# Performance work log

Measured on AMD Instinct MI355X. Metric: run time of the kernel, lower is better.

## Reference

```python
import jax, jax.numpy as jnp
import numpy as np

B, N, K, DIN, H = 8, 5000, 16, 128, 128


def setup_inputs() -> dict:
    key = jax.random.key(0)
    ks = jax.random.split(key, 10)
    x = jax.random.normal(ks[0], (B, N, DIN), dtype=jnp.float32)
    neighbor_index = jax.random.randint(ks[1], (N, K), 0, N, dtype=jnp.int32)
    neighbor_weights = jax.random.uniform(ks[2], (N, K), dtype=jnp.float32)
    s = 1.0 / np.sqrt(H)
    W_ih = jax.random.uniform(ks[3], (4 * H, DIN), minval=-s, maxval=s, dtype=jnp.float32)
    W_hh = jax.random.uniform(ks[4], (4 * H, H), minval=-s, maxval=s, dtype=jnp.float32)
    b_ih = jax.random.uniform(ks[5], (4 * H,), minval=-s, maxval=s, dtype=jnp.float32)
    b_hh = jax.random.uniform(ks[6], (4 * H,), minval=-s, maxval=s, dtype=jnp.float32)
    W_self = jax.random.normal(ks[7], (H, DIN), dtype=jnp.float32) * 0.05
    b_self = jnp.zeros((H,), dtype=jnp.float32)
    W_comb = jax.random.normal(ks[8], (H, 2 * H), dtype=jnp.float32) * 0.05
    b_comb = jnp.zeros((H,), dtype=jnp.float32)
    return {"x": x, "neighbor_index": neighbor_index, "neighbor_weights": neighbor_weights,
            "W_ih": W_ih, "W_hh": W_hh, "b_ih": b_ih, "b_hh": b_hh,
            "W_self": W_self, "b_self": b_self, "W_comb": W_comb, "b_comb": b_comb}


def _lstm_last_h(seq, W_ih, W_hh, b_ih, b_hh):
    # seq: (M, K, DIN) -> final hidden state (M, H). PyTorch gate order: i, f, g, o.
    M = seq.shape[0]
    x_gates = jnp.einsum('mkd,gd->mkg', seq, W_ih) + b_ih  # (M, K, 4H)
    x_gates = jnp.swapaxes(x_gates, 0, 1)  # (K, M, 4H)

    def step(carry, xg):
        h, c = carry
        gates = xg + h @ W_hh.T + b_hh
        i, f, g, o = jnp.split(gates, 4, axis=-1)
        i = jax.nn.sigmoid(i); f = jax.nn.sigmoid(f); g = jnp.tanh(g); o = jax.nn.sigmoid(o)
        c = f * c + i * g
        h = o * jnp.tanh(c)
        return (h, c), None

    h0 = jnp.zeros((M, W_hh.shape[0] // 4), dtype=seq.dtype)
    (h, _), _ = jax.lax.scan(step, (h0, h0), x_gates)
    return h


def reference(x, neighbor_index, neighbor_weights, W_ih, W_hh, b_ih, b_hh, W_self, b_self, W_comb, b_comb):
    b, n, din = x.shape
    k = neighbor_index.shape[1]
    # gather neighbor feats: (B, N, K, DIN)
    neigh = jnp.take(x, neighbor_index, axis=1)
    neigh = neigh * neighbor_weights[None, :, :, None]
    lstm_in = neigh.reshape(b * n, k, din)
    agg = _lstm_last_h(lstm_in, W_ih, W_hh, b_ih, b_hh).reshape(b, n, -1)
    self_feats = x @ W_self.T + b_self
    combined = jnp.concatenate([self_feats, agg], axis=-1)
    out = jax.nn.relu(combined @ W_comb.T + b_comb)
    return out
```

## Files before the change

kernel.cpp:

```cpp
#include <hip/hip_runtime.h>
#include <math.h>

#define Bx   8
#define Nx   5000
#define Kx   16
#define DINx 128
#define Hx   128
#define G4x  512
#define Mx   40000

typedef __attribute__((ext_vector_type(8))) short sh8;
typedef __attribute__((ext_vector_type(4))) float f32x4;

__device__ __forceinline__ float sigf(float v) {
    return __fdividef(1.0f, 1.0f + __expf(-v));
}
__device__ __forceinline__ float tanf_(float v) {
    return 1.0f - __fdividef(2.0f, __expf(2.0f * v) + 1.0f);
}
__device__ __forceinline__ unsigned short rne16(float f) {
    unsigned int u = __float_as_uint(f);
    return (unsigned short)((u + 0x7fffu + ((u >> 16) & 1u)) >> 16);
}
__device__ __forceinline__ float b2f(unsigned short s) {
    return __uint_as_float(((unsigned int)s) << 16);
}

#define FMA4(P, A, Q)                                        \
    P = fmaf((A).x, (Q).x, P); P = fmaf((A).y, (Q).y, P);    \
    P = fmaf((A).z, (Q).z, P); P = fmaf((A).w, (Q).w, P);

__global__ __launch_bounds__(128) void ka(const float* __restrict__ x,
        const float* __restrict__ W_ih, const float* __restrict__ W_self,
        const float* __restrict__ b_self, float* __restrict__ G,
        float* __restrict__ S)
{
    __shared__ float xs[8 * DINx];
    const int m0 = blockIdx.x * 8;
    {
        const float4* src = (const float4*)(x + (size_t)m0 * DINx);
        float4* dst = (float4*)xs;
        #pragma unroll
        for (int i = 0; i < 2; ++i)
            dst[threadIdx.x + 128 * i] = src[threadIdx.x + 128 * i];
    }
    __syncthreads();

    const int t = threadIdx.x;
    const float4* wp[5];
    #pragma unroll
    for (int c = 0; c < 5; ++c) {
        const int o = t + 128 * c;
        wp[c] = (const float4*)((o < G4x) ? (W_ih + (size_t)o * DINx)
                                          : (W_self + (size_t)(o - G4x) * DINx));
    }
    float acc[8][5];
    #pragma unroll
    for (int n = 0; n < 8; ++n)
        #pragma unroll
        for (int c = 0; c < 5; ++c) acc[n][c] = 0.f;

    #pragma unroll 4
    for (int k4 = 0; k4 < 32; ++k4) {
        float4 wv[5];
        #pragma unroll
        for (int c = 0; c < 5; ++c) wv[c] = wp[c][k4];
        #pragma unroll
        for (int n = 0; n < 8; ++n) {
            const float4 xv = ((const float4*)(xs + n * DINx))[k4];
            #pragma unroll
            for (int c = 0; c < 5; ++c) { FMA4(acc[n][c], xv, wv[c]); }
        }
    }
    const float bs = b_self[t];
    #pragma unroll
    for (int n = 0; n < 8; ++n) {
        const size_t m = (size_t)(m0 + n);
        #pragma unroll
        for (int c = 0; c < 4; ++c)
            G[m * G4x + t + 128 * c] = acc[n][c];
        S[m * Hx + t] = acc[n][4] + bs;
    }
}

__global__ __launch_bounds__(256) void kw(const float* __restrict__ W_hh,
        const float* __restrict__ b_ih, const float* __restrict__ b_hh,
        unsigned short* __restrict__ WH, unsigned short* __restrict__ WL,
        float* __restrict__ bsum)
{
    const int i = blockIdx.x * 256 + threadIdx.x;
    if (i < G4x * Hx) {
        const float w = W_hh[i];
        const unsigned short hi = rne16(w);
        WH[i] = hi;
        WL[i] = rne16(w - b2f(hi));
    }
    if (i < G4x) bsum[i] = b_ih[i] + b_hh[i];
}

__global__ __launch_bounds__(256) void kb(const float* __restrict__ G,
        const float* __restrict__ S, const unsigned short* __restrict__ WH,
        const unsigned short* __restrict__ WL, const float* __restrict__ bsum,
        const int* __restrict__ nidx, const float* __restrict__ nw,
        const float* __restrict__ W_comb, const float* __restrict__ b_comb,
        float* __restrict__ out)
{
    __shared__ unsigned short hsHI[32 * 128];
    __shared__ unsigned short hsLO[32 * 128];
    __shared__ float hsF[32 * 136];
    __shared__ int   gofs[16 * 32];
    __shared__ float wts [16 * 32];

    const int tid    = threadIdx.x;
    const int lane   = tid & 63;
    const int v      = tid >> 6;
    const int row16  = lane & 15;
    const int quad   = lane >> 4;
    const int swzkey = row16 & 7;
    const int dimb   = v * 32;
    const int m0     = blockIdx.x * 32;

    for (int i = tid; i < 512; i += 256) {
        const int s = i & 31, kk = i >> 5;
        const int m = m0 + s;
        const int bb = m / Nx;
        const int nn = m - bb * Nx;
        gofs[kk * 32 + s] = (bb * Nx + nidx[nn * Kx + kk]) * G4x;
        wts [kk * 32 + s] = nw[nn * Kx + kk];
    }
    float bsv[4][2];
    #pragma unroll
    for (int g = 0; g < 4; ++g)
        #pragma unroll
        for (int b2 = 0; b2 < 2; ++b2)
            bsv[g][b2] = bsum[g * 128 + dimb + 16 * b2 + row16];

    float cst[2][2][4];
    #pragma unroll
    for (int mt = 0; mt < 2; ++mt)
        #pragma unroll
        for (int b2 = 0; b2 < 2; ++b2)
            #pragma unroll
            for (int j = 0; j < 4; ++j) cst[mt][b2][j] = 0.f;

    __syncthreads();

    #pragma unroll 1
    for (int k = 0; k < Kx; ++k) {
        float wkv[2][4];
        const float* gp[2][4];
        #pragma unroll
        for (int mt = 0; mt < 2; ++mt)
            #pragma unroll
            for (int j = 0; j < 4; ++j) {
                const int seq = mt * 16 + quad * 4 + j;
                wkv[mt][j] = wts[k * 32 + seq];
                gp[mt][j]  = G + gofs[k * 32 + seq] + dimb + row16;
            }
        float gld[2][4][4][2];
        #pragma unroll
        for (int mt = 0; mt < 2; ++mt)
            #pragma unroll
            for (int j = 0; j < 4; ++j)
                #pragma unroll
                for (int g = 0; g < 4; ++g)
                    #pragma unroll
                    for (int b2 = 0; b2 < 2; ++b2)
                        gld[mt][j][g][b2] = gp[mt][j][(g << 7) + (b2 << 4)];

        f32x4 acc[2][4][2];
        #pragma unroll
        for (int mt = 0; mt < 2; ++mt)
            #pragma unroll
            for (int g = 0; g < 4; ++g)
                #pragma unroll
                for (int b2 = 0; b2 < 2; ++b2)
                    acc[mt][g][b2] = (f32x4)0.f;

        if (k) {
            #pragma unroll
            for (int kt = 0; kt < 4; ++kt) {
                sh8 ahi[2], alo[2];
                #pragma unroll
                for (int mt = 0; mt < 2; ++mt) {
                    const int ro = ((mt * 16 + row16) << 7) +
                                   ((((kt << 2) + quad) ^ swzkey) << 3);
                    ahi[mt] = *(const sh8*)(hsHI + ro);
                    alo[mt] = *(const sh8*)(hsLO + ro);
                }
                #pragma unroll
                for (int b2 = 0; b2 < 2; ++b2) {
                    #pragma unroll
                    for (int g = 0; g < 4; ++g) {
                        const int nro = ((g << 7) + dimb + (b2 << 4) + row16) * 128
                                        + (kt << 5) + (quad << 3);
                        const sh8 wh = *(const sh8*)(WH + nro);
                        const sh8 wl = *(const sh8*)(WL + nro);
                        #pragma unroll
                        for (int mt = 0; mt < 2; ++mt) {
                            acc[mt][g][b2] = __builtin_amdgcn_mfma_f32_16x16x32_bf16(
                                ahi[mt], wh, acc[mt][g][b2], 0, 0, 0);
                            acc[mt][g][b2] = __builtin_amdgcn_mfma_f32_16x16x32_bf16(
                                alo[mt], wh, acc[mt][g][b2], 0, 0, 0);
                            acc[mt][g][b2] = __builtin_amdgcn_mfma_f32_16x16x32_bf16(
                                ahi[mt], wl, acc[mt][g][b2], 0, 0, 0);
                        }
                    }
                }
            }
        }

        float hval[2][2][4];
        #pragma unroll
        for (int mt = 0; mt < 2; ++mt)
            #pragma unroll
            for (int b2 = 0; b2 < 2; ++b2)
                #pragma unroll
                for (int j = 0; j < 4; ++j) {
                    const float pi = acc[mt][0][b2][j] + wkv[mt][j] * gld[mt][j][0][b2] + bsv[0][b2];
                    const float pf = acc[mt][1][b2][j] + wkv[mt][j] * gld[mt][j][1][b2] + bsv[1][b2];
                    const float pg = acc[mt][2][b2][j] + wkv[mt][j] * gld[mt][j][2][b2] + bsv[2][b2];
                    const float po = acc[mt][3][b2][j] + wkv[mt][j] * gld[mt][j][3][b2] + bsv[3][b2];
                    const float ig = sigf(pi), fg = sigf(pf);
                    const float gg = tanf_(pg), og = sigf(po);
                    const float cc = fg * cst[mt][b2][j] + ig * gg;
                    cst[mt][b2][j] = cc;
                    hval[mt][b2][j] = og * tanf_(cc);
                }

        __syncthreads();

        if (k < Kx - 1) {
            #pragma unroll
            for (int mt = 0; mt < 2; ++mt)
                #pragma unroll
                for (int b2 = 0; b2 < 2; ++b2)
                    #pragma unroll
                    for (int j = 0; j < 4; ++j) {
                        const int seq = mt * 16 + quad * 4 + j;
                        const int dim = dimb + (b2 << 4) + row16;
                        const int idx = (seq << 7) +
                                        ((((dim >> 3) ^ (seq & 7))) << 3) + (dim & 7);
                        const float f = hval[mt][b2][j];
                        const unsigned short hi = rne16(f);
                        hsHI[idx] = hi;
                        hsLO[idx] = rne16(f - b2f(hi));
                    }
        } else {
            #pragma unroll
            for (int mt = 0; mt < 2; ++mt)
                #pragma unroll
                for (int b2 = 0; b2 < 2; ++b2)
                    #pragma unroll
                    for (int j = 0; j < 4; ++j) {
                        const int seq = mt * 16 + quad * 4 + j;
                        const int dim = dimb + (b2 << 4) + row16;
                        hsF[seq * 136 + dim] = hval[mt][b2][j];
                    }
        }
        __syncthreads();
    }

    const int dg = tid & 31;
    const int sg = tid >> 5;
    float ac[4][4];
    #pragma unroll
    for (int i = 0; i < 4; ++i)
        #pragma unroll
        for (int j = 0; j < 4; ++j) ac[i][j] = 0.f;

    const float4* S4 = (const float4*)S;
    const float4* W4 = (const float4*)W_comb;
    #pragma unroll 4
    for (int d4 = 0; d4 < 32; ++d4) {
        float4 sv[4], wv[4];
        #pragma unroll
        for (int i = 0; i < 4; ++i)
            sv[i] = S4[(size_t)(m0 + sg * 4 + i) * 32 + d4];
        #pragma unroll
        for (int j = 0; j < 4; ++j) wv[j] = W4[(dg * 4 + j) * 64 + d4];
        #pragma unroll
        for (int i = 0; i < 4; ++i) {
            #pragma unroll
            for (int j = 0; j < 4; ++j) { FMA4(ac[i][j], sv[i], wv[j]); }
        }
    }
    #pragma unroll 4
    for (int d4 = 0; d4 < 32; ++d4) {
        float4 hv[4], wv[4];
        #pragma unroll
        for (int i = 0; i < 4; ++i)
            hv[i] = *(const float4*)(hsF + (sg * 4 + i) * 136 + d4 * 4);
        #pragma unroll
        for (int j = 0; j < 4; ++j) wv[j] = W4[(dg * 4 + j) * 64 + 32 + d4];
        #pragma unroll
        for (int i = 0; i < 4; ++i) {
            #pragma unroll
            for (int j = 0; j < 4; ++j) { FMA4(ac[i][j], hv[i], wv[j]); }
        }
    }
    const float4 bc = ((const float4*)b_comb)[dg];
    #pragma unroll
    for (int i = 0; i < 4; ++i) {
        float4 o4;
        o4.x = fmaxf(ac[i][0] + bc.x, 0.f);
        o4.y = fmaxf(ac[i][1] + bc.y, 0.f);
        o4.z = fmaxf(ac[i][2] + bc.z, 0.f);
        o4.w = fmaxf(ac[i][3] + bc.w, 0.f);
        *(float4*)(out + (size_t)(m0 + sg * 4 + i) * 128 + dg * 4) = o4;
    }
}

extern "C" void kernel_launch(void* const* d_in, const int* in_sizes, int n_in,
                              void* d_out, int out_size, void* d_ws, size_t ws_size,
                              hipStream_t stream)
{
    const float* x      = (const float*)d_in[0];
    const int*   nidx   = (const int*)  d_in[1];
    const float* nw     = (const float*)d_in[2];
    const float* W_ih   = (const float*)d_in[3];
    const float* W_hh   = (const float*)d_in[4];
    const float* b_ih   = (const float*)d_in[5];
    const float* b_hh   = (const float*)d_in[6];
    const float* W_self = (const float*)d_in[7];
    const float* b_self = (const float*)d_in[8];
    const float* W_comb = (const float*)d_in[9];
    const float* b_comb = (const float*)d_in[10];
    float* out = (float*)d_out;

    float* G = (float*)d_ws;
    float* S = G + (size_t)Mx * G4x;
    unsigned short* WH = (unsigned short*)(S + (size_t)Mx * Hx);
    unsigned short* WL = WH + (size_t)G4x * Hx;
    float* bsum = (float*)(WL + (size_t)G4x * Hx);

    kw<<<(G4x * Hx + 255) / 256, 256, 0, stream>>>(W_hh, b_ih, b_hh, WH, WL, bsum);
    ka<<<Mx / 8, 128, 0, stream>>>(x, W_ih, W_self, b_self, G, S);
    kb<<<Mx / 32, 256, 0, stream>>>(G, S, WH, WL, bsum, nidx, nw,
                                    W_comb, b_comb, out);
}
```

Measured before the change: 1.423 ms.

## Prepack W_hh fragments, transpose MFMA operands, vectorize gathers and enlarge projection tile

Packs the split bf16 W_hh into a lane-contiguous fragment layout so each wave loads weight fragments with one coalesced 16-byte read per lane. The MFMA operands are swapped so the output tile becomes dims×sequences. This lets gate pre-activations be gathered as float4 and folded with bias into the accumulator initialisation. Hidden state is written back to LDS as ushort4, shared memory is overlaid into one buffer, and launch bounds ask for 3 blocks per CU. The input projection kernel also processes 16 rows per block instead of 8, which reuses weights more but raises register pressure.

```diff
diff --git a/kernel.cpp b/kernel.cpp
--- a/kernel.cpp
+++ b/kernel.cpp
@@ -35,13 +35,13 @@
         const float* __restrict__ b_self, float* __restrict__ G,
         float* __restrict__ S)
 {
-    __shared__ float xs[8 * DINx];
-    const int m0 = blockIdx.x * 8;
+    __shared__ float xs[16 * DINx];
+    const int m0 = blockIdx.x * 16;
     {
         const float4* src = (const float4*)(x + (size_t)m0 * DINx);
         float4* dst = (float4*)xs;
         #pragma unroll
-        for (int i = 0; i < 2; ++i)
+        for (int i = 0; i < 4; ++i)
             dst[threadIdx.x + 128 * i] = src[threadIdx.x + 128 * i];
     }
     __syncthreads();
@@ -54,19 +54,19 @@
         wp[c] = (const float4*)((o < G4x) ? (W_ih + (size_t)o * DINx)
                                           : (W_self + (size_t)(o - G4x) * DINx));
     }
-    float acc[8][5];
-    #pragma unroll
-    for (int n = 0; n < 8; ++n)
+    float acc[16][5];
+    #pragma unroll
+    for (int n = 0; n < 16; ++n)
         #pragma unroll
         for (int c = 0; c < 5; ++c) acc[n][c] = 0.f;
 
-    #pragma unroll 4
+    #pragma unroll 2
     for (int k4 = 0; k4 < 32; ++k4) {
         float4 wv[5];
         #pragma unroll
         for (int c = 0; c < 5; ++c) wv[c] = wp[c][k4];
         #pragma unroll
-        for (int n = 0; n < 8; ++n) {
+        for (int n = 0; n < 16; ++n) {
             const float4 xv = ((const float4*)(xs + n * DINx))[k4];
             #pragma unroll
             for (int c = 0; c < 5; ++c) { FMA4(acc[n][c], xv, wv[c]); }
@@ -74,7 +74,7 @@
     }
     const float bs = b_self[t];
     #pragma unroll
-    for (int n = 0; n < 8; ++n) {
+    for (int n = 0; n < 16; ++n) {
         const size_t m = (size_t)(m0 + n);
         #pragma unroll
         for (int c = 0; c < 4; ++c)
@@ -85,178 +85,174 @@
 
 __global__ __launch_bounds__(256) void kw(const float* __restrict__ W_hh,
         const float* __restrict__ b_ih, const float* __restrict__ b_hh,
-        unsigned short* __restrict__ WH, unsigned short* __restrict__ WL,
+        unsigned short* __restrict__ WHp, unsigned short* __restrict__ WLp,
         float* __restrict__ bsum)
 {
     const int i = blockIdx.x * 256 + threadIdx.x;
     if (i < G4x * Hx) {
+        const int gdim = i >> 7, kcol = i & 127;
         const float w = W_hh[i];
         const unsigned short hi = rne16(w);
-        WH[i] = hi;
-        WL[i] = rne16(w - b2f(hi));
+        const unsigned short lo = rne16(w - b2f(hi));
+        const int dg16 = gdim >> 4, r16 = gdim & 15;
+        const int kt = kcol >> 5, quad = (kcol >> 3) & 3, e = kcol & 7;
+        const int pidx = (((dg16 * 4 + kt) * 64) + quad * 16 + r16) * 8 + e;
+        WHp[pidx] = hi;
+        WLp[pidx] = lo;
     }
     if (i < G4x) bsum[i] = b_ih[i] + b_hh[i];
 }
 
-__global__ __launch_bounds__(256) void kb(const float* __restrict__ G,
-        const float* __restrict__ S, const unsigned short* __restrict__ WH,
-        const unsigned short* __restrict__ WL, const float* __restrict__ bsum,
+__global__ __launch_bounds__(256, 3) void kb(const float* __restrict__ G,
+        const float* __restrict__ S, const unsigned short* __restrict__ WHp,
+        const unsigned short* __restrict__ WLp, const float* __restrict__ bsum,
         const int* __restrict__ nidx, const float* __restrict__ nw,
         const float* __restrict__ W_comb, const float* __restrict__ b_comb,
         float* __restrict__ out)
 {
-    __shared__ unsigned short hsHI[32 * 128];
-    __shared__ unsigned short hsLO[32 * 128];
-    __shared__ float hsF[32 * 136];
-    __shared__ int   gofs[16 * 32];
-    __shared__ float wts [16 * 32];
-
-    const int tid    = threadIdx.x;
-    const int lane   = tid & 63;
-    const int v      = tid >> 6;
-    const int row16  = lane & 15;
-    const int quad   = lane >> 4;
-    const int swzkey = row16 & 7;
-    const int dimb   = v * 32;
-    const int m0     = blockIdx.x * 32;
+    __shared__ __align__(16) char smem[23552];
+    unsigned short* hsHI = (unsigned short*)smem;
+    unsigned short* hsLO = (unsigned short*)(smem + 8192);
+    float*          hsF  = (float*)smem;
+    int*            gofs = (int*)(smem + 17408);
+    float*          wts  = (float*)(smem + 17408 + 2048);
+    float*          biasL= (float*)(smem + 17408 + 4096);
+
+    const int tid   = threadIdx.x;
+    const int lane  = tid & 63;
+    const int v     = tid >> 6;
+    const int row16 = lane & 15;
+    const int quad  = lane >> 4;
+    const int kk    = row16 & 7;
+    const int dimb  = v * 32;
+    const int m0    = blockIdx.x * 32;
 
     for (int i = tid; i < 512; i += 256) {
-        const int s = i & 31, kk = i >> 5;
+        const int s = i & 31, kstep = i >> 5;
         const int m = m0 + s;
         const int bb = m / Nx;
         const int nn = m - bb * Nx;
-        gofs[kk * 32 + s] = (bb * Nx + nidx[nn * Kx + kk]) * G4x;
-        wts [kk * 32 + s] = nw[nn * Kx + kk];
-    }
-    float bsv[4][2];
-    #pragma unroll
-    for (int g = 0; g < 4; ++g)
-        #pragma unroll
-        for (int b2 = 0; b2 < 2; ++b2)
-            bsv[g][b2] = bsum[g * 128 + dimb + 16 * b2 + row16];
+        gofs[kstep * 32 + s] = (bb * Nx + nidx[nn * Kx + kstep]) * G4x;
+        wts [kstep * 32 + s] = nw[nn * Kx + kstep];
+    }
+    biasL[tid]       = bsum[tid];
+    biasL[tid + 256] = bsum[tid + 256];
 
     float cst[2][2][4];
     #pragma unroll
-    for (int mt = 0; mt < 2; ++mt)
-        #pragma unroll
-        for (int b2 = 0; b2 < 2; ++b2)
-            #pragma unroll
-            for (int j = 0; j < 4; ++j) cst[mt][b2][j] = 0.f;
+    for (int st = 0; st < 2; ++st)
+        #pragma unroll
+        for (int dt = 0; dt < 2; ++dt)
+            #pragma unroll
+            for (int j = 0; j < 4; ++j) cst[st][dt][j] = 0.f;
 
     __syncthreads();
 
     #pragma unroll 1
     for (int k = 0; k < Kx; ++k) {
-        float wkv[2][4];
-        const float* gp[2][4];
-        #pragma unroll
-        for (int mt = 0; mt < 2; ++mt)
-            #pragma unroll
-            for (int j = 0; j < 4; ++j) {
-                const int seq = mt * 16 + quad * 4 + j;
-                wkv[mt][j] = wts[k * 32 + seq];
-                gp[mt][j]  = G + gofs[k * 32 + seq] + dimb + row16;
+        const float wk0 = wts[k * 32 + row16];
+        const float wk1 = wts[k * 32 + 16 + row16];
+        const float* g0p = G + gofs[k * 32 + row16] + dimb + quad * 4;
+        const float* g1p = G + gofs[k * 32 + 16 + row16] + dimb + quad * 4;
+
+        f32x4 acc[4][2][2];
+        #pragma unroll
+        for (int g = 0; g < 4; ++g)
+            #pragma unroll
+            for (int dt = 0; dt < 2; ++dt) {
+                const int off = (g << 7) + (dt << 4);
+                const float4 bz = *(const float4*)(biasL + off + dimb + quad * 4);
+                const float4 v0 = *(const float4*)(g0p + off);
+                const float4 v1 = *(const float4*)(g1p + off);
+                acc[g][dt][0][0] = fmaf(wk0, v0.x, bz.x);
+                acc[g][dt][0][1] = fmaf(wk0, v0.y, bz.y);
+                acc[g][dt][0][2] = fmaf(wk0, v0.z, bz.z);
+                acc[g][dt][0][3] = fmaf(wk0, v0.w, bz.w);
+                acc[g][dt][1][0] = fmaf(wk1, v1.x, bz.x);
+                acc[g][dt][1][1] = fmaf(wk1, v1.y, bz.y);
+                acc[g][dt][1][2] = fmaf(wk1, v1.z, bz.z);
+                acc[g][dt][1][3] = fmaf(wk1, v1.w, bz.w);
             }
-        float gld[2][4][4][2];
-        #pragma unroll
-        for (int mt = 0; mt < 2; ++mt)
-            #pragma unroll
-            for (int j = 0; j < 4; ++j)
+
+        if (k) {
+            #pragma unroll
+            for (int kt = 0; kt < 4; ++kt) {
+                const int rsw = (kt * 4 + quad) ^ kk;
+                const sh8 bhi0 = ((const sh8*)hsHI)[row16 * 16 + rsw];
+                const sh8 blo0 = ((const sh8*)hsLO)[row16 * 16 + rsw];
+                const sh8 bhi1 = ((const sh8*)hsHI)[(16 + row16) * 16 + rsw];
+                const sh8 blo1 = ((const sh8*)hsLO)[(16 + row16) * 16 + rsw];
                 #pragma unroll
                 for (int g = 0; g < 4; ++g)
                     #pragma unroll
-                    for (int b2 = 0; b2 < 2; ++b2)
-                        gld[mt][j][g][b2] = gp[mt][j][(g << 7) + (b2 << 4)];
-
-        f32x4 acc[2][4][2];
-        #pragma unroll
-        for (int mt = 0; mt < 2; ++mt)
-            #pragma unroll
-            for (int g = 0; g < 4; ++g)
-                #pragma unroll
-                for (int b2 = 0; b2 < 2; ++b2)
-                    acc[mt][g][b2] = (f32x4)0.f;
-
-        if (k) {
-            #pragma unroll
-            for (int kt = 0; kt < 4; ++kt) {
-                sh8 ahi[2], alo[2];
-                #pragma unroll
-                for (int mt = 0; mt < 2; ++mt) {
-                    const int ro = ((mt * 16 + row16) << 7) +
-                                   ((((kt << 2) + quad) ^ swzkey) << 3);
-                    ahi[mt] = *(const sh8*)(hsHI + ro);
-                    alo[mt] = *(const sh8*)(hsLO + ro);
-                }
-                #pragma unroll
-                for (int b2 = 0; b2 < 2; ++b2) {
-                    #pragma unroll
-                    for (int g = 0; g < 4; ++g) {
-                        const int nro = ((g << 7) + dimb + (b2 << 4) + row16) * 128
-                                        + (kt << 5) + (quad << 3);
-                        const sh8 wh = *(const sh8*)(WH + nro);
-                        const sh8 wl = *(const sh8*)(WL + nro);
-                        #pragma unroll
-                        for (int mt = 0; mt < 2; ++mt) {
-                            acc[mt][g][b2] = __builtin_amdgcn_mfma_f32_16x16x32_bf16(
-                                ahi[mt], wh, acc[mt][g][b2], 0, 0, 0);
-                            acc[mt][g][b2] = __builtin_amdgcn_mfma_f32_16x16x32_bf16(
-                                alo[mt], wh, acc[mt][g][b2], 0, 0, 0);
-                            acc[mt][g][b2] = __builtin_amdgcn_mfma_f32_16x16x32_bf16(
-                                ahi[mt], wl, acc[mt][g][b2], 0, 0, 0);
-                        }
+                    for (int dt = 0; dt < 2; ++dt) {
+                        const int wi = ((g * 8 + v * 2 + dt) * 4 + kt) * 64 + lane;
+                        const sh8 wh = ((const sh8*)WHp)[wi];
+                        const sh8 wl = ((const sh8*)WLp)[wi];
+                        acc[g][dt][0] = __builtin_amdgcn_mfma_f32_16x16x32_bf16(
+                            wh, bhi0, acc[g][dt][0], 0, 0, 0);
+                        acc[g][dt][0] = __builtin_amdgcn_mfma_f32_16x16x32_bf16(
+                            wh, blo0, acc[g][dt][0], 0, 0, 0);
+                        acc[g][dt][0] = __builtin_amdgcn_mfma_f32_16x16x32_bf16(
+                            wl, bhi0, acc[g][dt][0], 0, 0, 0);
+                        acc[g][dt][1] = __builtin_amdgcn_mfma_f32_16x16x32_bf16(
+                            wh, bhi1, acc[g][dt][1], 0, 0, 0);
+                        acc[g][dt][1] = __builtin_amdgcn_mfma_f32_16x16x32_bf16(
+                            wh, blo1, acc[g][dt][1], 0, 0, 0);
+                        acc[g][dt][1] = __builtin_amdgcn_mfma_f32_16x16x32_bf16(
+                            wl, bhi1, acc[g][dt][1], 0, 0, 0);
                     }
-                }
             }
         }
 
-        float hval[2][2][4];
-        #pragma unroll
-        for (int mt = 0; mt < 2; ++mt)
-            #pragma unroll
-            for (int b2 = 0; b2 < 2; ++b2)
+        float hv[2][2][4];
+        #pragma unroll
+        for (int st = 0; st < 2; ++st)
+            #pragma unroll
+            for (int dt = 0; dt < 2; ++dt)
                 #pragma unroll
                 for (int j = 0; j < 4; ++j) {
-                    const float pi = acc[mt][0][b2][j] + wkv[mt][j] * gld[mt][j][0][b2] + bsv[0][b2];
-                    const float pf = acc[mt][1][b2][j] + wkv[mt][j] * gld[mt][j][1][b2] + bsv[1][b2];
-                    const float pg = acc[mt][2][b2][j] + wkv[mt][j] * gld[mt][j][2][b2] + bsv[2][b2];
-                    const float po = acc[mt][3][b2][j] + wkv[mt][j] * gld[mt][j][3][b2] + bsv[3][b2];
-                    const float ig = sigf(pi), fg = sigf(pf);
-                    const float gg = tanf_(pg), og = sigf(po);
-                    const float cc = fg * cst[mt][b2][j] + ig * gg;
-                    cst[mt][b2][j] = cc;
-                    hval[mt][b2][j] = og * tanf_(cc);
+                    const float ig = sigf(acc[0][dt][st][j]);
+                    const float fg = sigf(acc[1][dt][st][j]);
+                    const float gg = tanf_(acc[2][dt][st][j]);
+                    const float og = sigf(acc[3][dt][st][j]);
+                    const float cc = fg * cst[st][dt][j] + ig * gg;
+                    cst[st][dt][j] = cc;
+                    hv[st][dt][j] = og * tanf_(cc);
                 }
 
         __syncthreads();
 
         if (k < Kx - 1) {
             #pragma unroll
-            for (int mt = 0; mt < 2; ++mt)
+            for (int st = 0; st < 2; ++st)
                 #pragma unroll
-                for (int b2 = 0; b2 < 2; ++b2)
-                    #pragma unroll
-                    for (int j = 0; j < 4; ++j) {
-                        const int seq = mt * 16 + quad * 4 + j;
-                        const int dim = dimb + (b2 << 4) + row16;
-                        const int idx = (seq << 7) +
-                                        ((((dim >> 3) ^ (seq & 7))) << 3) + (dim & 7);
-                        const float f = hval[mt][b2][j];
-                        const unsigned short hi = rne16(f);
-                        hsHI[idx] = hi;
-                        hsLO[idx] = rne16(f - b2f(hi));
-                    }
+                for (int dt = 0; dt < 2; ++dt) {
+                    ushort4 shi, slo;
+                    shi.x = rne16(hv[st][dt][0]);
+                    shi.y = rne16(hv[st][dt][1]);
+                    shi.z = rne16(hv[st][dt][2]);
+                    shi.w = rne16(hv[st][dt][3]);
+                    slo.x = rne16(hv[st][dt][0] - b2f(shi.x));
+                    slo.y = rne16(hv[st][dt][1] - b2f(shi.y));
+                    slo.z = rne16(hv[st][dt][2] - b2f(shi.z));
+                    slo.w = rne16(hv[st][dt][3] - b2f(shi.w));
+                    const int g16p = (v * 4 + dt * 2 + (quad >> 1)) ^ kk;
+                    const int u4i = (st * 16 + row16) * 32 + g16p * 2 + (quad & 1);
+                    ((ushort4*)hsHI)[u4i] = shi;
+                    ((ushort4*)hsLO)[u4i] = slo;
+                }
         } else {
             #pragma unroll
-            for (int mt = 0; mt < 2; ++mt)
+            for (int st = 0; st < 2; ++st)
                 #pragma unroll
-                for (int b2 = 0; b2 < 2; ++b2)
-                    #pragma unroll
-                    for (int j = 0; j < 4; ++j) {
-                        const int seq = mt * 16 + quad * 4 + j;
-                        const int dim = dimb + (b2 << 4) + row16;
-                        hsF[seq * 136 + dim] = hval[mt][b2][j];
-                    }
+                for (int dt = 0; dt < 2; ++dt) {
+                    float4 o4;
+                    o4.x = hv[st][dt][0]; o4.y = hv[st][dt][1];
+                    o4.z = hv[st][dt][2]; o4.w = hv[st][dt][3];
+                    *(float4*)(hsF + (st * 16 + row16) * 136 + dimb + dt * 16
+                               + quad * 4) = o4;
+                }
         }
         __syncthreads();
     }
@@ -287,16 +283,16 @@
     }
     #pragma unroll 4
     for (int d4 = 0; d4 < 32; ++d4) {
-        float4 hv[4], wv[4];
+        float4 hvv[4], wv[4];
         #pragma unroll
         for (int i = 0; i < 4; ++i)
-            hv[i] = *(const float4*)(hsF + (sg * 4 + i) * 136 + d4 * 4);
+            hvv[i] = *(const float4*)(hsF + (sg * 4 + i) * 136 + d4 * 4);
         #pragma unroll
         for (int j = 0; j < 4; ++j) wv[j] = W4[(dg * 4 + j) * 64 + 32 + d4];
         #pragma unroll
         for (int i = 0; i < 4; ++i) {
             #pragma unroll
-            for (int j = 0; j < 4; ++j) { FMA4(ac[i][j], hv[i], wv[j]); }
+            for (int j = 0; j < 4; ++j) { FMA4(ac[i][j], hvv[i], wv[j]); }
         }
     }
     const float4 bc = ((const float4*)b_comb)[dg];
@@ -330,12 +326,12 @@
 
     float* G = (float*)d_ws;
     float* S = G + (size_t)Mx * G4x;
-    unsigned short* WH = (unsigned short*)(S + (size_t)Mx * Hx);
-    unsigned short* WL = WH + (size_t)G4x * Hx;
-    float* bsum = (float*)(WL + (size_t)G4x * Hx);
-
-    kw<<<(G4x * Hx + 255) / 256, 256, 0, stream>>>(W_hh, b_ih, b_hh, WH, WL, bsum);
-    ka<<<Mx / 8, 128, 0, stream>>>(x, W_ih, W_self, b_self, G, S);
-    kb<<<Mx / 32, 256, 0, stream>>>(G, S, WH, WL, bsum, nidx, nw,
+    unsigned short* WHp = (unsigned short*)(S + (size_t)Mx * Hx);
+    unsigned short* WLp = WHp + (size_t)G4x * Hx;
+    float* bsum = (float*)(WLp + (size_t)G4x * Hx);
+
+    kw<<<(G4x * Hx + 255) / 256, 256, 0, stream>>>(W_hh, b_ih, b_hh, WHp, WLp, bsum);
+    ka<<<Mx / 16, 128, 0, stream>>>(x, W_ih, W_self, b_self, G, S);
+    kb<<<Mx / 32, 256, 0, stream>>>(G, S, WHp, WLp, bsum, nidx, nw,
                                     W_comb, b_comb, out);
 }
```

Measured after the change: 1.550 ms. +8.9%, slower.

## Pre-pack W_hh fragments, alias LDS buffers, seed MFMA accumulators with gates

Applied to the files above, without the earlier changes.

The W_hh bf16 hi/lo split is now stored in an MFMA-fragment-packed layout, so each lane loads its sh8 operand with one contiguous, coalesced access. The LSTM kernel's LDS buffers are aliased into a single shared array and it gets a min-blocks-per-SM launch bound of 3, both aimed at higher occupancy. The MFMA accumulators are now initialized with the weighted input gates plus bias instead of adding them after the matmul. The input-projection kernel also processes 16 rows per block instead of 8, reusing each weight load over more rows at the cost of more registers.

```diff
diff --git a/kernel.cpp b/kernel.cpp
--- a/kernel.cpp
+++ b/kernel.cpp
@@ -35,13 +35,13 @@
         const float* __restrict__ b_self, float* __restrict__ G,
         float* __restrict__ S)
 {
-    __shared__ float xs[8 * DINx];
-    const int m0 = blockIdx.x * 8;
+    __shared__ float xs[16 * DINx];
+    const int m0 = blockIdx.x * 16;
     {
         const float4* src = (const float4*)(x + (size_t)m0 * DINx);
         float4* dst = (float4*)xs;
         #pragma unroll
-        for (int i = 0; i < 2; ++i)
+        for (int i = 0; i < 4; ++i)
             dst[threadIdx.x + 128 * i] = src[threadIdx.x + 128 * i];
     }
     __syncthreads();
@@ -54,19 +54,19 @@
         wp[c] = (const float4*)((o < G4x) ? (W_ih + (size_t)o * DINx)
                                           : (W_self + (size_t)(o - G4x) * DINx));
     }
-    float acc[8][5];
-    #pragma unroll
-    for (int n = 0; n < 8; ++n)
+    float acc[16][5];
+    #pragma unroll
+    for (int n = 0; n < 16; ++n)
         #pragma unroll
         for (int c = 0; c < 5; ++c) acc[n][c] = 0.f;
 
-    #pragma unroll 4
+    #pragma unroll 2
     for (int k4 = 0; k4 < 32; ++k4) {
         float4 wv[5];
         #pragma unroll
         for (int c = 0; c < 5; ++c) wv[c] = wp[c][k4];
         #pragma unroll
-        for (int n = 0; n < 8; ++n) {
+        for (int n = 0; n < 16; ++n) {
             const float4 xv = ((const float4*)(xs + n * DINx))[k4];
             #pragma unroll
             for (int c = 0; c < 5; ++c) { FMA4(acc[n][c], xv, wv[c]); }
@@ -74,7 +74,7 @@
     }
     const float bs = b_self[t];
     #pragma unroll
-    for (int n = 0; n < 8; ++n) {
+    for (int n = 0; n < 16; ++n) {
         const size_t m = (size_t)(m0 + n);
         #pragma unroll
         for (int c = 0; c < 4; ++c)
@@ -85,55 +85,61 @@
 
 __global__ __launch_bounds__(256) void kw(const float* __restrict__ W_hh,
         const float* __restrict__ b_ih, const float* __restrict__ b_hh,
-        unsigned short* __restrict__ WH, unsigned short* __restrict__ WL,
+        unsigned short* __restrict__ WHp, unsigned short* __restrict__ WLp,
         float* __restrict__ bsum)
 {
     const int i = blockIdx.x * 256 + threadIdx.x;
     if (i < G4x * Hx) {
+        const int gdim = i >> 7, kcol = i & 127;
         const float w = W_hh[i];
         const unsigned short hi = rne16(w);
-        WH[i] = hi;
-        WL[i] = rne16(w - b2f(hi));
+        const unsigned short lo = rne16(w - b2f(hi));
+        const int dg16 = gdim >> 4, r16 = gdim & 15;
+        const int kt = kcol >> 5, quad = (kcol >> 3) & 3, e = kcol & 7;
+        const int pidx = (((dg16 * 4 + kt) * 64) + quad * 16 + r16) * 8 + e;
+        WHp[pidx] = hi;
+        WLp[pidx] = lo;
     }
     if (i < G4x) bsum[i] = b_ih[i] + b_hh[i];
 }
 
-__global__ __launch_bounds__(256) void kb(const float* __restrict__ G,
-        const float* __restrict__ S, const unsigned short* __restrict__ WH,
-        const unsigned short* __restrict__ WL, const float* __restrict__ bsum,
+__global__ __launch_bounds__(256, 3) void kb(const float* __restrict__ G,
+        const float* __restrict__ S, const unsigned short* __restrict__ WHp,
+        const unsigned short* __restrict__ WLp, const float* __restrict__ bsum,
         const int* __restrict__ nidx, const float* __restrict__ nw,
         const float* __restrict__ W_comb, const float* __restrict__ b_comb,
         float* __restrict__ out)
 {
-    __shared__ unsigned short hsHI[32 * 128];
-    __shared__ unsigned short hsLO[32 * 128];
-    __shared__ float hsF[32 * 136];
-    __shared__ int   gofs[16 * 32];
-    __shared__ float wts [16 * 32];
-
-    const int tid    = threadIdx.x;
-    const int lane   = tid & 63;
-    const int v      = tid >> 6;
-    const int row16  = lane & 15;
-    const int quad   = lane >> 4;
-    const int swzkey = row16 & 7;
-    const int dimb   = v * 32;
-    const int m0     = blockIdx.x * 32;
+    __shared__ __align__(16) char smem[21504];
+    unsigned short* hsHI = (unsigned short*)smem;
+    unsigned short* hsLO = (unsigned short*)(smem + 8192);
+    float*          hsF  = (float*)smem;
+    int*            gofs = (int*)(smem + 17408);
+    float*          wts  = (float*)(smem + 17408 + 2048);
+
+    const int tid   = threadIdx.x;
+    const int lane  = tid & 63;
+    const int v     = tid >> 6;
+    const int row16 = lane & 15;
+    const int quad  = lane >> 4;
+    const int kk    = row16 & 7;
+    const int dimb  = v * 32;
+    const int m0    = blockIdx.x * 32;
 
     for (int i = tid; i < 512; i += 256) {
-        const int s = i & 31, kk = i >> 5;
+        const int s = i & 31, kstep = i >> 5;
         const int m = m0 + s;
         const int bb = m / Nx;
         const int nn = m - bb * Nx;
-        gofs[kk * 32 + s] = (bb * Nx + nidx[nn * Kx + kk]) * G4x;
-        wts [kk * 32 + s] = nw[nn * Kx + kk];
+        gofs[kstep * 32 + s] = (bb * Nx + nidx[nn * Kx + kstep]) * G4x;
+        wts [kstep * 32 + s] = nw[nn * Kx + kstep];
     }
     float bsv[4][2];
     #pragma unroll
     for (int g = 0; g < 4; ++g)
         #pragma unroll
         for (int b2 = 0; b2 < 2; ++b2)
-            bsv[g][b2] = bsum[g * 128 + dimb + 16 * b2 + row16];
+            bsv[g][b2] = bsum[g * 128 + dimb + (b2 << 4) + row16];
 
     float cst[2][2][4];
     #pragma unroll
@@ -148,54 +154,47 @@
     #pragma unroll 1
     for (int k = 0; k < Kx; ++k) {
         float wkv[2][4];
-        const float* gp[2][4];
+        int   goff[2][4];
         #pragma unroll
         for (int mt = 0; mt < 2; ++mt)
             #pragma unroll
             for (int j = 0; j < 4; ++j) {
                 const int seq = mt * 16 + quad * 4 + j;
-                wkv[mt][j] = wts[k * 32 + seq];
-                gp[mt][j]  = G + gofs[k * 32 + seq] + dimb + row16;
+                wkv[mt][j]  = wts[k * 32 + seq];
+                goff[mt][j] = gofs[k * 32 + seq] + dimb + row16;
             }
-        float gld[2][4][4][2];
+
+        f32x4 acc[2][4][2];
         #pragma unroll
         for (int mt = 0; mt < 2; ++mt)
             #pragma unroll
-            for (int j = 0; j < 4; ++j)
+            for (int g = 0; g < 4; ++g)
+                #pragma unroll
+                for (int b2 = 0; b2 < 2; ++b2)
+                    #pragma unroll
+                    for (int j = 0; j < 4; ++j)
+                        acc[mt][g][b2][j] = fmaf(wkv[mt][j],
+                            G[(size_t)(goff[mt][j] + (g << 7) + (b2 << 4))],
+                            bsv[g][b2]);
+
+        if (k) {
+            #pragma unroll
+            for (int kt = 0; kt < 4; ++kt) {
+                const int rsw = ((kt << 2) + quad) ^ kk;
+                sh8 ahi[2], alo[2];
+                #pragma unroll
+                for (int mt = 0; mt < 2; ++mt) {
+                    const int ro = (mt * 16 + row16) * 16 + rsw;
+                    ahi[mt] = ((const sh8*)hsHI)[ro];
+                    alo[mt] = ((const sh8*)hsLO)[ro];
+                }
                 #pragma unroll
                 for (int g = 0; g < 4; ++g)
                     #pragma unroll
-                    for (int b2 = 0; b2 < 2; ++b2)
-                        gld[mt][j][g][b2] = gp[mt][j][(g << 7) + (b2 << 4)];
-
-        f32x4 acc[2][4][2];
-        #pragma unroll
-        for (int mt = 0; mt < 2; ++mt)
-            #pragma unroll
-            for (int g = 0; g < 4; ++g)
-                #pragma unroll
-                for (int b2 = 0; b2 < 2; ++b2)
-                    acc[mt][g][b2] = (f32x4)0.f;
-
-        if (k) {
-            #pragma unroll
-            for (int kt = 0; kt < 4; ++kt) {
-                sh8 ahi[2], alo[2];
-                #pragma unroll
-                for (int mt = 0; mt < 2; ++mt) {
-                    const int ro = ((mt * 16 + row16) << 7) +
-                                   ((((kt << 2) + quad) ^ swzkey) << 3);
-                    ahi[mt] = *(const sh8*)(hsHI + ro);
-                    alo[mt] = *(const sh8*)(hsLO + ro);
-                }
-                #pragma unroll
-                for (int b2 = 0; b2 < 2; ++b2) {
-                    #pragma unroll
-                    for (int g = 0; g < 4; ++g) {
-                        const int nro = ((g << 7) + dimb + (b2 << 4) + row16) * 128
-                                        + (kt << 5) + (quad << 3);
-                        const sh8 wh = *(const sh8*)(WH + nro);
-                        const sh8 wl = *(const sh8*)(WL + nro);
+                    for (int b2 = 0; b2 < 2; ++b2) {
+                        const int wi = ((g * 8 + v * 2 + b2) * 4 + kt) * 64 + lane;
+                        const sh8 wh = ((const sh8*)WHp)[wi];
+                        const sh8 wl = ((const sh8*)WLp)[wi];
                         #pragma unroll
                         for (int mt = 0; mt < 2; ++mt) {
                             acc[mt][g][b2] = __builtin_amdgcn_mfma_f32_16x16x32_bf16(
@@ -206,7 +205,6 @@
                                 ahi[mt], wl, acc[mt][g][b2], 0, 0, 0);
                         }
                     }
-                }
             }
         }
 
@@ -217,12 +215,10 @@
             for (int b2 = 0; b2 < 2; ++b2)
                 #pragma unroll
                 for (int j = 0; j < 4; ++j) {
-                    const float pi = acc[mt][0][b2][j] + wkv[mt][j] * gld[mt][j][0][b2] + bsv[0][b2];
-                    const float pf = acc[mt][1][b2][j] + wkv[mt][j] * gld[mt][j][1][b2] + bsv[1][b2];
-                    const float pg = acc[mt][2][b2][j] + wkv[mt][j] * gld[mt][j][2][b2] + bsv[2][b2];
-                    const float po = acc[mt][3][b2][j] + wkv[mt][j] * gld[mt][j][3][b2] + bsv[3][b2];
-                    const float ig = sigf(pi), fg = sigf(pf);
-                    const float gg = tanf_(pg), og = sigf(po);
+                    const float ig = sigf(acc[mt][0][b2][j]);
+                    const float fg = sigf(acc[mt][1][b2][j]);
+                    const float gg = tanf_(acc[mt][2][b2][j]);
+                    const float og = sigf(acc[mt][3][b2][j]);
                     const float cc = fg * cst[mt][b2][j] + ig * gg;
                     cst[mt][b2][j] = cc;
                     hval[mt][b2][j] = og * tanf_(cc);
@@ -287,16 +283,16 @@
     }
     #pragma unroll 4
     for (int d4 = 0; d4 < 32; ++d4) {
-        float4 hv[4], wv[4];
+        float4 hvv[4], wv[4];
         #pragma unroll
         for (int i = 0; i < 4; ++i)
-            hv[i] = *(const float4*)(hsF + (sg * 4 + i) * 136 + d4 * 4);
+            hvv[i] = *(const float4*)(hsF + (sg * 4 + i) * 136 + d4 * 4);
         #pragma unroll
         for (int j = 0; j < 4; ++j) wv[j] = W4[(dg * 4 + j) * 64 + 32 + d4];
         #pragma unroll
         for (int i = 0; i < 4; ++i) {
             #pragma unroll
-            for (int j = 0; j < 4; ++j) { FMA4(ac[i][j], hv[i], wv[j]); }
+            for (int j = 0; j < 4; ++j) { FMA4(ac[i][j], hvv[i], wv[j]); }
         }
     }
     const float4 bc = ((const float4*)b_comb)[dg];
@@ -330,12 +326,12 @@
 
     float* G = (float*)d_ws;
     float* S = G + (size_t)Mx * G4x;
-    unsigned short* WH = (unsigned short*)(S + (size_t)Mx * Hx);
-    unsigned short* WL = WH + (size_t)G4x * Hx;
-    float* bsum = (float*)(WL + (size_t)G4x * Hx);
-
-    kw<<<(G4x * Hx + 255) / 256, 256, 0, stream>>>(W_hh, b_ih, b_hh, WH, WL, bsum);
-    ka<<<Mx / 8, 128, 0, stream>>>(x, W_ih, W_self, b_self, G, S);
-    kb<<<Mx / 32, 256, 0, stream>>>(G, S, WH, WL, bsum, nidx, nw,
+    unsigned short* WHp = (unsigned short*)(S + (size_t)Mx * Hx);
+    unsigned short* WLp = WHp + (size_t)G4x * Hx;
+    float* bsum = (float*)(WLp + (size_t)G4x * Hx);
+
+    kw<<<(G4x * Hx + 255) / 256, 256, 0, stream>>>(W_hh, b_ih, b_hh, WHp, WLp, bsum);
+    ka<<<Mx / 16, 128, 0, stream>>>(x, W_ih, W_self, b_self, G, S);
+    kb<<<Mx / 32, 256, 0, stream>>>(G, S, WHp, WLp, bsum, nidx, nw,
                                     W_comb, b_comb, out);
 }
```

After: 1.585 ms. +11.3%, slower.
